# Performance work log

Hardware: AMD Instinct MI355X
Metric: run time of the kernel (lower is better)

Reference implementation:

```python
import jax, jax.numpy as jnp
import numpy as np

BS = 256      # number of graphs
NODES = 128   # nodes per graph (equal-size segments)
N = BS * NODES
D = 64        # node feature dim
C = 64        # codebook atoms
K = 32        # support points per atom


def setup_inputs() -> dict:
    key = jax.random.key(0)
    k1, k2 = jax.random.split(key)
    x = jax.random.normal(k1, (N, D), dtype=jnp.float32)
    atoms = jax.random.normal(k2, (C, K, D), dtype=jnp.float32)
    batch = jnp.repeat(jnp.arange(BS, dtype=jnp.int64), NODES)  # sorted graph ids
    return {"x": x, "atoms": atoms, "batch": batch, "bs": BS}


def _sq_dists(a, b):
    # a: [..., n, D], b: [..., m, D] -> [..., n, m] squared euclidean distances
    an = jnp.sum(a * a, axis=-1)
    bn = jnp.sum(b * b, axis=-1)
    ab = jnp.einsum('...nd,...md->...nm', a, b)
    return an[..., :, None] + bn[..., None, :] - 2.0 * ab


def reference(x, atoms, batch, bs):
    # Faithful vectorized version of GINSWDSingleModel._mmd_distances with
    # gamma = 1/D (default). Assumes equal-size graphs (batch = repeat(arange(bs), n)).
    Nn, Dd = x.shape
    Cc, Kk, _ = atoms.shape
    n = Nn // bs
    gamma = 1.0 / Dd
    xg = x.reshape(bs, n, Dd)                      # [bs, n, D]

    # k_xx: within-graph RBF kernel mean, per graph -> [bs]
    k_xx = jnp.exp(-gamma * _sq_dists(xg, xg)).mean(axis=(1, 2))

    # k_yy: within-atom kernel mean, per atom -> [C]
    k_yy = jnp.exp(-gamma * _sq_dists(atoms, atoms)).mean(axis=(1, 2))

    # k_xy: cross kernel mean between graph nodes and atom points -> [bs, C]
    xn = jnp.sum(xg * xg, axis=-1)                 # [bs, n]
    an = jnp.sum(atoms * atoms, axis=-1)           # [C, K]
    xa = jnp.einsum('bnd,ckd->bnck', xg, atoms)    # [bs, n, C, K]
    dxy = xn[:, :, None, None] + an[None, None, :, :] - 2.0 * xa
    k_xy = jnp.exp(-gamma * dxy).mean(axis=(1, 3))  # [bs, C]

    return k_xx[:, None] + k_yy[None, :] - 2.0 * k_xy
```

## Files before the change

### kernel.cpp

```cpp
#include <hip/hip_runtime.h>
#include <hip/hip_bf16.h>


constexpr int   NODES = 128;
constexpr int   DD    = 64;
constexpr int   CC    = 64;
constexpr int   KK    = 32;
constexpr float GAMMA = 1.0f / 64.0f;
constexpr float LOG2E = 1.4426950408889634f;
constexpr float C1    = 2.0f * GAMMA * LOG2E;
constexpr float GL    = GAMMA * LOG2E;

typedef __attribute__((ext_vector_type(8)))  short short8;
typedef __attribute__((ext_vector_type(16))) float f32x16;

#define MFMA(a, b, c) __builtin_amdgcn_mfma_f32_32x32x16_bf16((a), (b), (c), 0, 0, 0)

__device__ __forceinline__ float fexp2(float x) {
    float r;
    asm("v_exp_f32 %0, %1" : "=v"(r) : "v"(x));
    return r;
}

__device__ __forceinline__ unsigned short f2bf(float f) {
    union { float f; unsigned int u; } a; a.f = f;
    unsigned int u = a.u;
    return (unsigned short)((u + 0x7FFFu + ((u >> 16) & 1u)) >> 16);
}

__device__ __forceinline__ void gl16(const void* g, void* l) {
    __builtin_amdgcn_global_load_lds(
        (const __attribute__((address_space(1))) char*)g,
        (__attribute__((address_space(3))) char*)l, 16, 0, 0);
}

__device__ __forceinline__ float epi16(const f32x16 acc, const f32x16 cx) {
    float sa = 0.f, sb = 0.f;
#pragma unroll
    for (int r = 0; r < 16; r += 2) {
        sa += fexp2(fmaf(C1, acc[r],     cx[r]));
        sb += fexp2(fmaf(C1, acc[r + 1], cx[r + 1]));
    }
    return sa + sb;
}

__global__ __launch_bounds__(256) void prep_x(const float* __restrict__ x,
                                              short8* __restrict__ xfrag,
                                              float* __restrict__ nrm) {
    const int b = blockIdx.x, t = threadIdx.x;
    __shared__ float a[NODES][DD + 1];

    const float4* xg = reinterpret_cast<const float4*>(x + (size_t)b * NODES * DD);
    for (int i = t; i < NODES * DD / 4; i += 256) {
        const float4 v = xg[i];
        const int r = i >> 4, c4 = (i & 15) * 4;
        a[r][c4 + 0] = v.x; a[r][c4 + 1] = v.y;
        a[r][c4 + 2] = v.z; a[r][c4 + 3] = v.w;
    }
    __syncthreads();

    if (t < NODES) {
        float s = 0.f;
#pragma unroll
        for (int d = 0; d < DD; ++d) s = fmaf(a[t][d], a[t][d], s);
        nrm[b * NODES + t] = -GL * s;
    }

#pragma unroll
    for (int j = 0; j < 4; ++j) {
        const int e = t + 256 * j;
        const int l = e & 63, sl = e >> 6;
        const int row = (sl >> 2) * 32 + (l & 31);
        const int k0  = (sl & 3) * 16 + (l >> 5) * 8;
        short8 h;
#pragma unroll
        for (int q = 0; q < 8; ++q) h[q] = (short)f2bf(a[row][k0 + q]);
        xfrag[(size_t)b * 1024 + e] = h;
    }
}

__global__ __launch_bounds__(256) void prep_atoms(const float* __restrict__ atoms,
                                                  short8* __restrict__ bfrag,
                                                  float* __restrict__ eck,
                                                  float* __restrict__ kyy) {
    const int c = blockIdx.x, t = threadIdx.x;
    __shared__ float a[KK][DD + 1];
    __shared__ float an[KK];
    __shared__ float wred[4];

    const float* ac = atoms + (size_t)c * KK * DD;
    for (int i = t; i < KK * DD; i += 256) a[i >> 6][i & 63] = ac[i];
    __syncthreads();

    if (t < KK) {
        float s = 0.f;
#pragma unroll
        for (int d = 0; d < DD; ++d) s = fmaf(a[t][d], a[t][d], s);
        an[t] = s;
        eck[c * KK + t] = fexp2(-GL * s);
    }
    __syncthreads();

    {
        const int wv = t >> 6, l = t & 63;
        const int kp = l & 31, khh = l >> 5;
        short8 h;
#pragma unroll
        for (int j = 0; j < 8; ++j) h[j] = (short)f2bf(a[kp][wv * 16 + khh * 8 + j]);
        bfrag[((size_t)c * 4 + wv) * 64 + l] = h;
    }

    {
        const int i = t >> 3, j0 = (t & 7) * 4;
        float s0 = 0, s1 = 0, s2 = 0, s3 = 0;
        for (int d = 0; d < DD; ++d) {
            const float aid = a[i][d];
            s0 = fmaf(aid, a[j0 + 0][d], s0);
            s1 = fmaf(aid, a[j0 + 1][d], s1);
            s2 = fmaf(aid, a[j0 + 2][d], s2);
            s3 = fmaf(aid, a[j0 + 3][d], s3);
        }
        const float ani = an[i];
        float s = fexp2(-GL * (ani + an[j0 + 0] - 2.f * s0))
                + fexp2(-GL * (ani + an[j0 + 1] - 2.f * s1))
                + fexp2(-GL * (ani + an[j0 + 2] - 2.f * s2))
                + fexp2(-GL * (ani + an[j0 + 3] - 2.f * s3));
#pragma unroll
        for (int off = 32; off; off >>= 1) s += __shfl_xor(s, off);
        if ((t & 63) == 0) wred[t >> 6] = s;
    }
    __syncthreads();
    if (t == 0) kyy[c] = (wred[0] + wred[1] + wred[2] + wred[3]) * (1.0f / (KK * KK));
}

__global__ __launch_bounds__(256, 4) void mmd_fused(const short8* __restrict__ xfrag,
                                                    const short8* __restrict__ bfrag,
                                                    const float* __restrict__ nrm,
                                                    const float* __restrict__ eck,
                                                    float* __restrict__ kxxp,
                                                    float* __restrict__ sxyw) {
    const int bid = blockIdx.x, b = bid >> 2, cq = bid & 3;
    const int t = threadIdx.x, w = t >> 6, l = t & 63;
    const int l31 = l & 31, kh = l >> 5, rh = w >> 1, aq = w & 1;

    __shared__ short8 Bb[2][2][256];
    __shared__ short8 Bx[256];
    __shared__ float  part16[4][9][16];

    const short8* xa = xfrag + (size_t)b * 1024;
    short8 A0[4], A1[4];
#pragma unroll
    for (int kt = 0; kt < 4; ++kt) {
        A0[kt] = xa[((2 * rh) * 4 + kt) * 64 + l];
        A1[kt] = xa[((2 * rh + 1) * 4 + kt) * 64 + l];
    }

    f32x16 cx0, cx1;
    {
        const float* nb = nrm + b * NODES + (2 * rh) * 32 + 4 * kh;
#pragma unroll
        for (int q = 0; q < 4; ++q) {
            const float4 v0 = *reinterpret_cast<const float4*>(nb + 8 * q);
            const float4 v1 = *reinterpret_cast<const float4*>(nb + 32 + 8 * q);
            cx0[4*q+0] = v0.x; cx0[4*q+1] = v0.y; cx0[4*q+2] = v0.z; cx0[4*q+3] = v0.w;
            cx1[4*q+0] = v1.x; cx1[4*q+1] = v1.y; cx1[4*q+2] = v1.z; cx1[4*q+3] = v1.w;
        }
    }
    const float ec0 = fexp2(nrm[b * NODES + cq * 32 + l31]);

    gl16(xa + ((size_t)cq * 4 + w) * 64 + l, &Bx[w * 64]);
    __syncthreads();

    const short8* bq = bfrag + (size_t)(cq * 16) * 4 * 64;
    const int tsw = rh, si0 = aq * 2;

    {
        const short8* src = bq + ((size_t)(tsw * 8 + 0) * 4) * 64;
        gl16(src + (si0    ) * 64 + l, &Bb[1][tsw][(si0    ) * 64]);
        gl16(src + (si0 + 1) * 64 + l, &Bb[1][tsw][(si0 + 1) * 64]);

        short8 Bt[4];
#pragma unroll
        for (int kt = 0; kt < 4; ++kt) Bt[kt] = Bx[kt * 64 + l];
        f32x16 acc = {};
        if (aq == 0) {
#pragma unroll
            for (int kt = 0; kt < 4; ++kt) acc = MFMA(A0[kt], Bt[kt], acc);
        } else {
#pragma unroll
            for (int kt = 0; kt < 4; ++kt) acc = MFMA(A1[kt], Bt[kt], acc);
        }
        float s = epi16(acc, aq ? cx1 : cx0) * ec0;
        s += __shfl_xor(s, 32);
        s += __shfl_xor(s, 16);
        if (l < 16) part16[w][8][l] = s;
        __syncthreads();
    }

    for (int it = 1; it <= 8; ++it) {
        if (it < 8) {
            const short8* src = bq + ((size_t)(tsw * 8 + it) * 4) * 64;
            gl16(src + (si0    ) * 64 + l, &Bb[(it + 1) & 1][tsw][(si0    ) * 64]);
            gl16(src + (si0 + 1) * 64 + l, &Bb[(it + 1) & 1][tsw][(si0 + 1) * 64]);
        }
        short8 Bt[4];
#pragma unroll
        for (int kt = 0; kt < 4; ++kt) Bt[kt] = Bb[it & 1][aq][kt * 64 + l];

        f32x16 a0 = {}, a1 = {};
#pragma unroll
        for (int kt = 0; kt < 4; ++kt) {
            a0 = MFMA(A0[kt], Bt[kt], a0);
            a1 = MFMA(A1[kt], Bt[kt], a1);
        }
        const float ec = eck[(cq * 16 + aq * 8 + it - 1) * KK + l31];
        float s = (epi16(a0, cx0) + epi16(a1, cx1)) * ec;
        s += __shfl_xor(s, 32);
        s += __shfl_xor(s, 16);
        if (l < 16) part16[w][it - 1][l] = s;
        __syncthreads();
    }

    {
        const int o = t >> 4, g = t & 15;
        const int aqo = o >> 3, ito = o & 7;
        float s = part16[aqo][ito][g] + part16[2 + aqo][ito][g];
        s += __shfl_xor(s, 8);
        s += __shfl_xor(s, 4);
        s += __shfl_xor(s, 2);
        s += __shfl_xor(s, 1);
        if (g == 0) sxyw[b * CC + cq * 16 + aqo * 8 + ito] = s;
    }
    if (t < 16) {
        float s = part16[0][8][t] + part16[1][8][t]
                + part16[2][8][t] + part16[3][8][t];
        s += __shfl_xor(s, 8);
        s += __shfl_xor(s, 4);
        s += __shfl_xor(s, 2);
        s += __shfl_xor(s, 1);
        if (t == 0) kxxp[b * 4 + cq] = s;
    }
}

__global__ __launch_bounds__(256) void combine(const float* __restrict__ kxxp,
                                               const float* __restrict__ kyy,
                                               const float* __restrict__ sxyw,
                                               float* __restrict__ out) {
    const int idx = blockIdx.x * 256 + threadIdx.x;
    const int b = idx >> 6, c = idx & 63;
    const float kxx = (kxxp[b * 4 + 0] + kxxp[b * 4 + 1] +
                       kxxp[b * 4 + 2] + kxxp[b * 4 + 3]) * (1.0f / 16384.0f);
    out[idx] = kxx + kyy[c] - sxyw[idx] * (1.0f / 2048.0f);
}

extern "C" void kernel_launch(void* const* d_in, const int* in_sizes, int n_in,
                              void* d_out, int out_size, void* d_ws, size_t ws_size,
                              hipStream_t stream) {
    const float* x     = (const float*)d_in[0];
    const float* atoms = (const float*)d_in[1];
    float* out = (float*)d_out;

    char* ws = (char*)d_ws;
    short8* xfrag = (short8*)(ws);
    short8* bfrag = (short8*)(ws + 4194304);
    float*  nrm   = (float*) (ws + 4456448);
    float*  eck   = (float*) (ws + 4587520);
    float*  kyy   = (float*) (ws + 4595712);
    float*  kxxp  = (float*) (ws + 4595968);
    float*  sxyw  = (float*) (ws + 4600064);

    prep_x    <<<dim3(256),  dim3(256), 0, stream>>>(x, xfrag, nrm);
    prep_atoms<<<dim3(CC),   dim3(256), 0, stream>>>(atoms, bfrag, eck, kyy);
    mmd_fused <<<dim3(1024), dim3(256), 0, stream>>>(xfrag, bfrag, nrm, eck, kxxp, sxyw);
    combine   <<<dim3(CC),   dim3(256), 0, stream>>>(kxxp, kyy, sxyw, out);
}
```

Before: 32.73 us.

## Merge prep kernels and restructure mmd loop into fewer, larger pipelined stages

Merges the two preprocessing kernels into one launch with 320 blocks, each block branching on its index to handle either x or atoms, so one kernel launch goes away. In the main kernel, each stage now loads two atom tiles per wave into a wider double buffer and runs 4 stages instead of 8. That halves the number of __syncthreads barriers. Node norms are staged in shared memory and the per-atom scale factors are preloaded into registers, replacing the per-iteration global loads. The cost is more LDS per block and register pressure that could reduce occupancy.

```diff
diff --git a/kernel.cpp b/kernel.cpp
--- a/kernel.cpp
+++ b/kernel.cpp
@@ -34,103 +34,96 @@
         (__attribute__((address_space(3))) char*)l, 16, 0, 0);
 }
 
-__device__ __forceinline__ float epi16(const f32x16 acc, const f32x16 cx) {
-    float sa = 0.f, sb = 0.f;
-#pragma unroll
-    for (int r = 0; r < 16; r += 2) {
-        sa += fexp2(fmaf(C1, acc[r],     cx[r]));
-        sb += fexp2(fmaf(C1, acc[r + 1], cx[r + 1]));
-    }
-    return sa + sb;
-}
-
-__global__ __launch_bounds__(256) void prep_x(const float* __restrict__ x,
-                                              short8* __restrict__ xfrag,
-                                              float* __restrict__ nrm) {
-    const int b = blockIdx.x, t = threadIdx.x;
-    __shared__ float a[NODES][DD + 1];
-
-    const float4* xg = reinterpret_cast<const float4*>(x + (size_t)b * NODES * DD);
-    for (int i = t; i < NODES * DD / 4; i += 256) {
-        const float4 v = xg[i];
-        const int r = i >> 4, c4 = (i & 15) * 4;
-        a[r][c4 + 0] = v.x; a[r][c4 + 1] = v.y;
-        a[r][c4 + 2] = v.z; a[r][c4 + 3] = v.w;
-    }
-    __syncthreads();
-
-    if (t < NODES) {
-        float s = 0.f;
-#pragma unroll
-        for (int d = 0; d < DD; ++d) s = fmaf(a[t][d], a[t][d], s);
-        nrm[b * NODES + t] = -GL * s;
-    }
-
-#pragma unroll
-    for (int j = 0; j < 4; ++j) {
-        const int e = t + 256 * j;
-        const int l = e & 63, sl = e >> 6;
-        const int row = (sl >> 2) * 32 + (l & 31);
-        const int k0  = (sl & 3) * 16 + (l >> 5) * 8;
-        short8 h;
-#pragma unroll
-        for (int q = 0; q < 8; ++q) h[q] = (short)f2bf(a[row][k0 + q]);
-        xfrag[(size_t)b * 1024 + e] = h;
-    }
-}
-
-__global__ __launch_bounds__(256) void prep_atoms(const float* __restrict__ atoms,
-                                                  short8* __restrict__ bfrag,
-                                                  float* __restrict__ eck,
-                                                  float* __restrict__ kyy) {
-    const int c = blockIdx.x, t = threadIdx.x;
-    __shared__ float a[KK][DD + 1];
-    __shared__ float an[KK];
-    __shared__ float wred[4];
-
-    const float* ac = atoms + (size_t)c * KK * DD;
-    for (int i = t; i < KK * DD; i += 256) a[i >> 6][i & 63] = ac[i];
-    __syncthreads();
-
-    if (t < KK) {
-        float s = 0.f;
-#pragma unroll
-        for (int d = 0; d < DD; ++d) s = fmaf(a[t][d], a[t][d], s);
-        an[t] = s;
-        eck[c * KK + t] = fexp2(-GL * s);
-    }
-    __syncthreads();
-
-    {
-        const int wv = t >> 6, l = t & 63;
-        const int kp = l & 31, khh = l >> 5;
-        short8 h;
-#pragma unroll
-        for (int j = 0; j < 8; ++j) h[j] = (short)f2bf(a[kp][wv * 16 + khh * 8 + j]);
-        bfrag[((size_t)c * 4 + wv) * 64 + l] = h;
-    }
-
-    {
-        const int i = t >> 3, j0 = (t & 7) * 4;
-        float s0 = 0, s1 = 0, s2 = 0, s3 = 0;
-        for (int d = 0; d < DD; ++d) {
-            const float aid = a[i][d];
-            s0 = fmaf(aid, a[j0 + 0][d], s0);
-            s1 = fmaf(aid, a[j0 + 1][d], s1);
-            s2 = fmaf(aid, a[j0 + 2][d], s2);
-            s3 = fmaf(aid, a[j0 + 3][d], s3);
-        }
-        const float ani = an[i];
-        float s = fexp2(-GL * (ani + an[j0 + 0] - 2.f * s0))
-                + fexp2(-GL * (ani + an[j0 + 1] - 2.f * s1))
-                + fexp2(-GL * (ani + an[j0 + 2] - 2.f * s2))
-                + fexp2(-GL * (ani + an[j0 + 3] - 2.f * s3));
-#pragma unroll
-        for (int off = 32; off; off >>= 1) s += __shfl_xor(s, off);
-        if ((t & 63) == 0) wred[t >> 6] = s;
-    }
-    __syncthreads();
-    if (t == 0) kyy[c] = (wred[0] + wred[1] + wred[2] + wred[3]) * (1.0f / (KK * KK));
+__global__ __launch_bounds__(256) void prep(const float* __restrict__ x,
+                                            const float* __restrict__ atoms,
+                                            short8* __restrict__ xfrag,
+                                            float* __restrict__ nrm,
+                                            short8* __restrict__ bfrag,
+                                            float* __restrict__ eck,
+                                            float* __restrict__ kyy) {
+    __shared__ float smem[NODES * (DD + 1)];
+    const int bid = blockIdx.x, t = threadIdx.x;
+
+    if (bid < 256) {
+        const int b = bid;
+        float (*a)[DD + 1] = (float(*)[DD + 1])smem;
+
+        const float4* xg = reinterpret_cast<const float4*>(x + (size_t)b * NODES * DD);
+        for (int i = t; i < NODES * DD / 4; i += 256) {
+            const float4 v = xg[i];
+            const int r = i >> 4, c4 = (i & 15) * 4;
+            a[r][c4 + 0] = v.x; a[r][c4 + 1] = v.y;
+            a[r][c4 + 2] = v.z; a[r][c4 + 3] = v.w;
+        }
+        __syncthreads();
+
+        if (t < NODES) {
+            float s = 0.f;
+#pragma unroll
+            for (int d = 0; d < DD; ++d) s = fmaf(a[t][d], a[t][d], s);
+            nrm[b * NODES + t] = -GL * s;
+        }
+#pragma unroll
+        for (int j = 0; j < 4; ++j) {
+            const int e = t + 256 * j;
+            const int l = e & 63, sl = e >> 6;
+            const int row = (sl >> 2) * 32 + (l & 31);
+            const int k0  = (sl & 3) * 16 + (l >> 5) * 8;
+            short8 h;
+#pragma unroll
+            for (int q = 0; q < 8; ++q) h[q] = (short)f2bf(a[row][k0 + q]);
+            xfrag[(size_t)b * 1024 + e] = h;
+        }
+    } else {
+        const int c = bid - 256;
+        float (*a)[DD + 1] = (float(*)[DD + 1])smem;
+        float* an   = smem + KK * (DD + 1);
+        float* wred = an + KK;
+
+        const float* ac = atoms + (size_t)c * KK * DD;
+        for (int i = t; i < KK * DD; i += 256) a[i >> 6][i & 63] = ac[i];
+        __syncthreads();
+
+        if (t < KK) {
+            float s = 0.f;
+#pragma unroll
+            for (int d = 0; d < DD; ++d) s = fmaf(a[t][d], a[t][d], s);
+            an[t] = s;
+            eck[c * KK + t] = fexp2(-GL * s);
+        }
+        __syncthreads();
+
+        {
+            const int wv = t >> 6, l = t & 63;
+            const int kp = l & 31, khh = l >> 5;
+            short8 h;
+#pragma unroll
+            for (int j = 0; j < 8; ++j) h[j] = (short)f2bf(a[kp][wv * 16 + khh * 8 + j]);
+            bfrag[(size_t)c * 256 + wv * 64 + l] = h;
+        }
+
+        {
+            const int i = t >> 3, j0 = (t & 7) * 4;
+            float s0 = 0, s1 = 0, s2 = 0, s3 = 0;
+            for (int d = 0; d < DD; ++d) {
+                const float aid = a[i][d];
+                s0 = fmaf(aid, a[j0 + 0][d], s0);
+                s1 = fmaf(aid, a[j0 + 1][d], s1);
+                s2 = fmaf(aid, a[j0 + 2][d], s2);
+                s3 = fmaf(aid, a[j0 + 3][d], s3);
+            }
+            const float ani = an[i];
+            float s = fexp2(-GL * (ani + an[j0 + 0] - 2.f * s0))
+                    + fexp2(-GL * (ani + an[j0 + 1] - 2.f * s1))
+                    + fexp2(-GL * (ani + an[j0 + 2] - 2.f * s2))
+                    + fexp2(-GL * (ani + an[j0 + 3] - 2.f * s3));
+#pragma unroll
+            for (int off = 32; off; off >>= 1) s += __shfl_xor(s, off);
+            if ((t & 63) == 0) wred[t >> 6] = s;
+        }
+        __syncthreads();
+        if (t == 0) kyy[c] = (wred[0] + wred[1] + wred[2] + wred[3]) * (1.0f / (KK * KK));
+    }
 }
 
 __global__ __launch_bounds__(256, 4) void mmd_fused(const short8* __restrict__ xfrag,
@@ -143,9 +136,10 @@
     const int t = threadIdx.x, w = t >> 6, l = t & 63;
     const int l31 = l & 31, kh = l >> 5, rh = w >> 1, aq = w & 1;
 
-    __shared__ short8 Bb[2][2][256];
+    __shared__ short8 Bb[2][4][256];
     __shared__ short8 Bx[256];
     __shared__ float  part16[4][9][16];
+    __shared__ float  nl[NODES];
 
     const short8* xa = xfrag + (size_t)b * 1024;
     short8 A0[4], A1[4];
@@ -155,69 +149,90 @@
         A1[kt] = xa[((2 * rh + 1) * 4 + kt) * 64 + l];
     }
 
-    f32x16 cx0, cx1;
-    {
-        const float* nb = nrm + b * NODES + (2 * rh) * 32 + 4 * kh;
-#pragma unroll
-        for (int q = 0; q < 4; ++q) {
-            const float4 v0 = *reinterpret_cast<const float4*>(nb + 8 * q);
-            const float4 v1 = *reinterpret_cast<const float4*>(nb + 32 + 8 * q);
-            cx0[4*q+0] = v0.x; cx0[4*q+1] = v0.y; cx0[4*q+2] = v0.z; cx0[4*q+3] = v0.w;
-            cx1[4*q+0] = v1.x; cx1[4*q+1] = v1.y; cx1[4*q+2] = v1.z; cx1[4*q+3] = v1.w;
-        }
-    }
-    const float ec0 = fexp2(nrm[b * NODES + cq * 32 + l31]);
+    if (t < NODES) nl[t] = nrm[b * NODES + t];
+
+    float ecv[8];
+#pragma unroll
+    for (int j = 0; j < 8; ++j)
+        ecv[j] = eck[(cq * 16 + aq * 8 + j) * KK + l31];
 
     gl16(xa + ((size_t)cq * 4 + w) * 64 + l, &Bx[w * 64]);
     __syncthreads();
 
-    const short8* bq = bfrag + (size_t)(cq * 16) * 4 * 64;
-    const int tsw = rh, si0 = aq * 2;
-
-    {
-        const short8* src = bq + ((size_t)(tsw * 8 + 0) * 4) * 64;
-        gl16(src + (si0    ) * 64 + l, &Bb[1][tsw][(si0    ) * 64]);
-        gl16(src + (si0 + 1) * 64 + l, &Bb[1][tsw][(si0 + 1) * 64]);
-
-        short8 Bt[4];
-#pragma unroll
-        for (int kt = 0; kt < 4; ++kt) Bt[kt] = Bx[kt * 64 + l];
-        f32x16 acc = {};
-        if (aq == 0) {
-#pragma unroll
-            for (int kt = 0; kt < 4; ++kt) acc = MFMA(A0[kt], Bt[kt], acc);
+    const float ec0 = fexp2(nl[cq * 32 + l31]);
+    const float* nbase = &nl[(2 * rh) * 32 + 4 * kh];
+    const short8* bq = bfrag + (size_t)(cq * 16) * 256;
+
+#pragma unroll
+    for (int s = 0; s <= 4; ++s) {
+        if (s < 4) {
+            const int ct = (w >> 1) * 8 + 2 * s + (w & 1);
+            const short8* src = bq + (size_t)ct * 256;
+#pragma unroll
+            for (int q = 0; q < 4; ++q)
+                gl16(src + q * 64 + l, &Bb[s & 1][w][q * 64]);
+        }
+
+        if (s == 0) {
+            short8 Bt[4];
+#pragma unroll
+            for (int kt = 0; kt < 4; ++kt) Bt[kt] = Bx[kt * 64 + l];
+            f32x16 acc = {};
+            if (aq == 0) {
+#pragma unroll
+                for (int kt = 0; kt < 4; ++kt) acc = MFMA(A0[kt], Bt[kt], acc);
+            } else {
+#pragma unroll
+                for (int kt = 0; kt < 4; ++kt) acc = MFMA(A1[kt], Bt[kt], acc);
+            }
+            float ssum = 0.f;
+            const float* nb = &nl[(2 * rh + aq) * 32 + 4 * kh];
+#pragma unroll
+            for (int q = 0; q < 4; ++q) {
+                const float4 cn = *reinterpret_cast<const float4*>(nb + 8 * q);
+                ssum += fexp2(fmaf(C1, acc[4 * q + 0], cn.x));
+                ssum += fexp2(fmaf(C1, acc[4 * q + 1], cn.y));
+                ssum += fexp2(fmaf(C1, acc[4 * q + 2], cn.z));
+                ssum += fexp2(fmaf(C1, acc[4 * q + 3], cn.w));
+            }
+            ssum *= ec0;
+            ssum += __shfl_xor(ssum, 32);
+            ssum += __shfl_xor(ssum, 16);
+            if (l < 16) part16[w][8][l] = ssum;
         } else {
-#pragma unroll
-            for (int kt = 0; kt < 4; ++kt) acc = MFMA(A1[kt], Bt[kt], acc);
-        }
-        float s = epi16(acc, aq ? cx1 : cx0) * ec0;
-        s += __shfl_xor(s, 32);
-        s += __shfl_xor(s, 16);
-        if (l < 16) part16[w][8][l] = s;
-        __syncthreads();
-    }
-
-    for (int it = 1; it <= 8; ++it) {
-        if (it < 8) {
-            const short8* src = bq + ((size_t)(tsw * 8 + it) * 4) * 64;
-            gl16(src + (si0    ) * 64 + l, &Bb[(it + 1) & 1][tsw][(si0    ) * 64]);
-            gl16(src + (si0 + 1) * 64 + l, &Bb[(it + 1) & 1][tsw][(si0 + 1) * 64]);
-        }
-        short8 Bt[4];
-#pragma unroll
-        for (int kt = 0; kt < 4; ++kt) Bt[kt] = Bb[it & 1][aq][kt * 64 + l];
-
-        f32x16 a0 = {}, a1 = {};
-#pragma unroll
-        for (int kt = 0; kt < 4; ++kt) {
-            a0 = MFMA(A0[kt], Bt[kt], a0);
-            a1 = MFMA(A1[kt], Bt[kt], a1);
-        }
-        const float ec = eck[(cq * 16 + aq * 8 + it - 1) * KK + l31];
-        float s = (epi16(a0, cx0) + epi16(a1, cx1)) * ec;
-        s += __shfl_xor(s, 32);
-        s += __shfl_xor(s, 16);
-        if (l < 16) part16[w][it - 1][l] = s;
+            const int set = s - 1, buf = set & 1;
+#pragma unroll
+            for (int p = 0; p < 2; ++p) {
+                short8 Bt[4];
+#pragma unroll
+                for (int kt = 0; kt < 4; ++kt)
+                    Bt[kt] = Bb[buf][aq * 2 + p][kt * 64 + l];
+                f32x16 a0 = {}, a1 = {};
+#pragma unroll
+                for (int kt = 0; kt < 4; ++kt) {
+                    a0 = MFMA(A0[kt], Bt[kt], a0);
+                    a1 = MFMA(A1[kt], Bt[kt], a1);
+                }
+                float sA = 0.f, sB = 0.f;
+#pragma unroll
+                for (int q = 0; q < 4; ++q) {
+                    const float4 cA = *reinterpret_cast<const float4*>(nbase + 8 * q);
+                    const float4 cB = *reinterpret_cast<const float4*>(nbase + 32 + 8 * q);
+                    sA += fexp2(fmaf(C1, a0[4 * q + 0], cA.x));
+                    sA += fexp2(fmaf(C1, a0[4 * q + 1], cA.y));
+                    sA += fexp2(fmaf(C1, a0[4 * q + 2], cA.z));
+                    sA += fexp2(fmaf(C1, a0[4 * q + 3], cA.w));
+                    sB += fexp2(fmaf(C1, a1[4 * q + 0], cB.x));
+                    sB += fexp2(fmaf(C1, a1[4 * q + 1], cB.y));
+                    sB += fexp2(fmaf(C1, a1[4 * q + 2], cB.z));
+                    sB += fexp2(fmaf(C1, a1[4 * q + 3], cB.w));
+                }
+                float ssum = (sA + sB) * ecv[2 * set + p];
+                ssum += __shfl_xor(ssum, 32);
+                ssum += __shfl_xor(ssum, 16);
+                if (l < 16) part16[w][2 * set + p][l] = ssum;
+            }
+        }
         __syncthreads();
     }
 
@@ -269,8 +284,7 @@
     float*  kxxp  = (float*) (ws + 4595968);
     float*  sxyw  = (float*) (ws + 4600064);
 
-    prep_x    <<<dim3(256),  dim3(256), 0, stream>>>(x, xfrag, nrm);
-    prep_atoms<<<dim3(CC),   dim3(256), 0, stream>>>(atoms, bfrag, eck, kyy);
+    prep      <<<dim3(320),  dim3(256), 0, stream>>>(x, atoms, xfrag, nrm, bfrag, eck, kyy);
     mmd_fused <<<dim3(1024), dim3(256), 0, stream>>>(xfrag, bfrag, nrm, eck, kxxp, sxyw);
     combine   <<<dim3(CC),   dim3(256), 0, stream>>>(kxxp, kyy, sxyw, out);
 }
```

Result: faster. 29.52 us (-9.8%).
